# Kernel optimization log

Measured on AMD Instinct MI355X. Metric: run time of the kernel, lower is better.

The kernel has to match this reference:

```python
import jax, jax.numpy as jnp
import numpy as np

X_DIM = 64
Y_DIM = 64
U_DIM = 64
BATCH = 32
SEQ_LEN = 2048
DT = 1.0 / 1024.0
EPS = 1e-4


def setup_inputs() -> dict:
    key = jax.random.key(0)
    k_y, k_a, k_c = jax.random.split(key, 3)
    y = jax.random.normal(k_y, (BATCH, SEQ_LEN, Y_DIM), dtype=jnp.float32)
    # parameters, matching the module's initialization (small noise added to A/C for generality)
    A = jnp.diag(-0.01 * (jnp.arange(X_DIM, dtype=jnp.float32) + 1.0)) \
        + 0.001 * jax.random.normal(k_a, (X_DIM, X_DIM), dtype=jnp.float32)
    B = jnp.eye(X_DIM, U_DIM, dtype=jnp.float32) * 0.1
    C = 0.1 * jax.random.normal(k_c, (Y_DIM, X_DIM), dtype=jnp.float32)
    L_Q = jnp.eye(X_DIM, dtype=jnp.float32) * 0.316
    L_R = jnp.eye(U_DIM, dtype=jnp.float32) * 0.316
    L_V = jnp.eye(Y_DIM, dtype=jnp.float32)
    L_Q_proc = jnp.eye(X_DIM, dtype=jnp.float32) * 0.1
    x0_mean = jnp.zeros((X_DIM,), dtype=jnp.float32)
    P0 = jnp.eye(X_DIM, dtype=jnp.float32) * 0.1
    return {"y": y, "A": A, "B": B, "C": C, "L_Q": L_Q, "L_R": L_R,
            "L_V": L_V, "L_Q_proc": L_Q_proc, "x0_mean": x0_mean, "P0": P0}


def _riccati_step(S, H, n):
    # Euler step of the augmented Hamiltonian flow; P = V @ U^{-1}
    S_new = S + DT * (H @ S)
    U, V = S_new[:n], S_new[n:]
    X = V @ jnp.linalg.inv(U)
    return X, S_new


def _forward(y, A, B, C, L_Q, L_R, L_V, L_Q_proc, x0_mean, P0):
    n = A.shape[0]
    u_dim = B.shape[1]
    y_dim = C.shape[0]
    batch, seq_len, _ = y.shape

    Q = L_Q @ L_Q.T
    R = L_R @ L_R.T
    V = L_V @ L_V.T
    Q_proc = L_Q_proc @ L_Q_proc.T

    # normalize observations (torch.std is unbiased -> ddof=1)
    y_mean = y.mean(axis=(0, 1), keepdims=True)
    y_std = y.std(axis=(0, 1), keepdims=True, ddof=1)
    yn = (y - y_mean) / (y_std + EPS)

    # --- LQR Riccati recursion: P_seq, K_seq (sequential scan over time) ---
    R_inv_reg = jnp.linalg.inv(R + EPS * jnp.eye(u_dim, dtype=R.dtype))
    H_care = jnp.block([[A, -B @ jnp.linalg.inv(R) @ B.T],
                        [-Q, -A.T]])  # augmented Hamiltonian (2n, 2n)

    def lqr_step(S, _):
        X, S_new = _riccati_step(S, H_care, n)
        P = 0.5 * (X + X.T)
        K = R_inv_reg @ (B.T @ P)  # (u_dim, n)
        return S_new, (P, K)

    S0 = jnp.concatenate([jnp.eye(n, dtype=Q.dtype), Q], axis=0)  # P0 = Q
    _, (P_seq, K_seq) = jax.lax.scan(lqr_step, S0, None, length=seq_len)

    # --- Kalman filter (sequential scan, data-dependent per-step linear algebra) ---
    V_reg = V + EPS * jnp.eye(y_dim, dtype=V.dtype)
    V_chol = jnp.linalg.cholesky(V_reg)
    log_det_V = 2.0 * jnp.sum(jnp.log(jnp.diagonal(V_chol)))
    Z = jnp.zeros((n, n), dtype=A.dtype)
    LOG_2PI = jnp.log(2.0 * jnp.pi).astype(A.dtype)

    def kf_step(carry, inp):
        x_t, S, ll = carry
        K_t, y_t = inp  # (u_dim, n), (batch, y_dim)
        A_eff = A - B @ K_t
        x_pred = x_t + DT * (x_t @ A_eff.T)  # (batch, n)
        H_t = jnp.block([[A_eff, Q_proc], [Z, -A_eff.T]])
        P_new, S = _riccati_step(S, H_t, n)
        P_pred = 0.5 * (P_new + P_new.T)
        residual = y_t - x_pred @ C.T  # (batch, y_dim)
        CtP = C @ P_pred  # (y_dim, n)
        Sm = CtP @ C.T + V
        S_inv = jnp.linalg.inv(Sm + EPS * jnp.eye(y_dim, dtype=Sm.dtype))
        Kg = CtP.T @ S_inv  # (n, y_dim)
        x_new = x_pred + residual @ Kg.T
        quad = jnp.sum(residual * (residual @ S_inv.T))  # sum_b r^T S_inv r
        ll = ll - 0.5 * (quad + log_det_V + y_dim * LOG_2PI)
        return (x_new, S, ll), x_new

    S0_kf = jnp.concatenate([jnp.eye(n, dtype=P0.dtype), P0], axis=0)
    x0 = jnp.broadcast_to(x0_mean, (batch, n))
    y_t_major = jnp.swapaxes(yn, 0, 1)  # (T, B, y_dim)
    (_, _, ll), x_filt_t = jax.lax.scan(kf_step, (x0, S0_kf, jnp.float32(0.0)),
                                        (K_seq, y_t_major))
    x_filt = jnp.swapaxes(x_filt_t, 0, 1)  # (B, T, n)
    log_likelihood = ll / seq_len

    # controls, prediction, quadratic costs (fully vectorized)
    u_seq = -jnp.einsum('tux,btx->btu', K_seq, x_filt)
    y_pred = x_filt @ C.T
    x_cost = jnp.einsum('btx,xz,btz->b', x_filt, Q, x_filt)
    u_cost = jnp.einsum('btu,uv,btv->b', u_seq, R, u_seq)
    control_cost = jnp.mean(x_cost + u_cost)
    return log_likelihood, control_cost, x_filt, u_seq, y_pred, yn


def reference(y, A, B, C, L_Q, L_R, L_V, L_Q_proc, x0_mean, P0):
    return _forward(y, A, B, C, L_Q, L_R, L_V, L_Q_proc, x0_mean, P0)
```

## Files before the change

kernel.cpp:

```cpp
#include <hip/hip_runtime.h>
#include <math.h>

#define XD 64
#define SEQL 2048
#define NB 32
#define DT_C  (1.0f/1024.0f)
#define EPS_C 1e-4f
#define LD 68
#define PLD 136
#define LOG2PI 1.8378770664093453f
#define CHUNK 16
#define NCH 128

#define OFF_PARTIAL 0u
#define OFF_MEAN    32768u
#define OFF_STD     32832u
#define OFF_Q       32896u
#define OFF_R       36992u
#define OFF_VM      41088u
#define OFF_QP      45184u
#define OFF_RIREG   49280u
#define OFF_LOGDET  53376u
#define OFF_CHAIN   53440u
#define OFF_POW     250048u
#define OFF_BOUNDS  1298624u
#define OFF_K       1568960u
#define OFF_AEFF    9957568u
#define OFF_UV      18346176u
#define OFF_G       35123392u
#define OFF_B       43512000u
#define OFF_OPS2    47706304u
#define OFF_OPS3G   50852032u
#define OFF_OPS3B   51900608u
#define OFF_SB2     52424896u
#define OFF_XB      53473472u
#define OFF_QUAD    53735616u
#define OFF_COST    53737664u

#define OOFF_XF 2
#define OOFF_U  4194306
#define OOFF_YP 8388610
#define OOFF_YN 12582914

template<int KD>
__device__ __forceinline__ void mmNN(int t, float* __restrict__ out, int ldo,
    const float* __restrict__ A, int lda, const float* __restrict__ B, int ldb,
    const float* __restrict__ addC = nullptr, int ldc = 0, float alpha = 1.0f)
{
  const int r0 = (t >> 4) << 2, c0 = (t & 15) << 2;
  float acc[4][4] = {};
  for (int k = 0; k < KD; k += 4) {
    float a_[4][4];
    #pragma unroll
    for (int i = 0; i < 4; ++i) {
      const float4 x = *(const float4*)&A[(r0+i)*lda + k];
      a_[i][0]=x.x; a_[i][1]=x.y; a_[i][2]=x.z; a_[i][3]=x.w;
    }
    #pragma unroll
    for (int kk = 0; kk < 4; ++kk) {
      const float4 bv = *(const float4*)&B[(k+kk)*ldb + c0];
      #pragma unroll
      for (int i = 0; i < 4; ++i) {
        const float a = a_[i][kk];
        acc[i][0] += a*bv.x; acc[i][1] += a*bv.y; acc[i][2] += a*bv.z; acc[i][3] += a*bv.w;
      }
    }
  }
  #pragma unroll
  for (int i = 0; i < 4; ++i)
    #pragma unroll
    for (int j = 0; j < 4; ++j) {
      float v = alpha*acc[i][j];
      if (addC) v += addC[(r0+i)*ldc + (c0+j)];
      out[(r0+i)*ldo + (c0+j)] = v;
    }
}

template<int KD>
__device__ __forceinline__ void mmTA(int t, float* __restrict__ out, int ldo,
    const float* __restrict__ A, int lda, const float* __restrict__ B, int ldb,
    const float* __restrict__ addC = nullptr, int ldc = 0, float alpha = 1.0f)
{
  const int r0 = (t >> 4) << 2, c0 = (t & 15) << 2;
  float acc[4][4] = {};
  for (int k = 0; k < KD; k += 4) {
    #pragma unroll
    for (int kk = 0; kk < 4; ++kk) {
      const float4 av4 = *(const float4*)&A[(k+kk)*lda + r0];
      const float4 bv4 = *(const float4*)&B[(k+kk)*ldb + c0];
      const float av[4] = {av4.x, av4.y, av4.z, av4.w};
      const float bv[4] = {bv4.x, bv4.y, bv4.z, bv4.w};
      #pragma unroll
      for (int i = 0; i < 4; ++i)
        #pragma unroll
        for (int j = 0; j < 4; ++j)
          acc[i][j] += av[i]*bv[j];
    }
  }
  #pragma unroll
  for (int i = 0; i < 4; ++i)
    #pragma unroll
    for (int j = 0; j < 4; ++j) {
      float v = alpha*acc[i][j];
      if (addC) v += addC[(r0+i)*ldc + (c0+j)];
      out[(r0+i)*ldo + (c0+j)] = v;
    }
}

template<int KD>
__device__ __forceinline__ void mmTB(int t, float* __restrict__ out, int ldo,
    const float* __restrict__ A, int lda, const float* __restrict__ B, int ldb,
    const float* __restrict__ addC = nullptr, int ldc = 0, float alpha = 1.0f)
{
  const int r0 = (t >> 4) << 2, c0 = (t & 15) << 2;
  float acc[4][4] = {};
  for (int k = 0; k < KD; k += 4) {
    float a_[4][4], b_[4][4];
    #pragma unroll
    for (int i = 0; i < 4; ++i) {
      const float4 x = *(const float4*)&A[(r0+i)*lda + k];
      a_[i][0]=x.x; a_[i][1]=x.y; a_[i][2]=x.z; a_[i][3]=x.w;
    }
    #pragma unroll
    for (int j = 0; j < 4; ++j) {
      const float4 x = *(const float4*)&B[(c0+j)*ldb + k];
      b_[j][0]=x.x; b_[j][1]=x.y; b_[j][2]=x.z; b_[j][3]=x.w;
    }
    #pragma unroll
    for (int i = 0; i < 4; ++i)
      #pragma unroll
      for (int j = 0; j < 4; ++j)
        acc[i][j] += a_[i][0]*b_[j][0] + a_[i][1]*b_[j][1] + a_[i][2]*b_[j][2] + a_[i][3]*b_[j][3];
  }
  #pragma unroll
  for (int i = 0; i < 4; ++i)
    #pragma unroll
    for (int j = 0; j < 4; ++j) {
      float v = alpha*acc[i][j];
      if (addC) v += addC[(r0+i)*ldc + (c0+j)];
      out[(r0+i)*ldo + (c0+j)] = v;
    }
}

template<int KD>
__device__ __forceinline__ void mm32NN(int t, float* __restrict__ out, int ldo,
    const float* __restrict__ A, int lda, const float* __restrict__ B, int ldb,
    const float* __restrict__ addC = nullptr, int ldc = 0, float alpha = 1.0f)
{
  const int r0 = (t >> 4) << 1, c0 = (t & 15) << 2;
  float acc[2][4] = {};
  for (int k = 0; k < KD; k += 4) {
    float a_[2][4];
    #pragma unroll
    for (int i = 0; i < 2; ++i) {
      const float4 x = *(const float4*)&A[(r0+i)*lda + k];
      a_[i][0]=x.x; a_[i][1]=x.y; a_[i][2]=x.z; a_[i][3]=x.w;
    }
    #pragma unroll
    for (int kk = 0; kk < 4; ++kk) {
      const float4 bv = *(const float4*)&B[(k+kk)*ldb + c0];
      #pragma unroll
      for (int i = 0; i < 2; ++i) {
        const float a = a_[i][kk];
        acc[i][0] += a*bv.x; acc[i][1] += a*bv.y; acc[i][2] += a*bv.z; acc[i][3] += a*bv.w;
      }
    }
  }
  #pragma unroll
  for (int i = 0; i < 2; ++i)
    #pragma unroll
    for (int j = 0; j < 4; ++j) {
      float v = alpha*acc[i][j];
      if (addC) v += addC[(r0+i)*ldc + (c0+j)];
      out[(r0+i)*ldo + (c0+j)] = v;
    }
}

template<int KD>
__device__ __forceinline__ void mm32TB(int t, float* __restrict__ out, int ldo,
    const float* __restrict__ A, int lda, const float* __restrict__ B, int ldb,
    const float* __restrict__ addC = nullptr, int ldc = 0, float alpha = 1.0f)
{
  const int r0 = (t >> 4) << 1, c0 = (t & 15) << 2;
  float acc[2][4] = {};
  for (int k = 0; k < KD; k += 4) {
    float a_[2][4], b_[4][4];
    #pragma unroll
    for (int i = 0; i < 2; ++i) {
      const float4 x = *(const float4*)&A[(r0+i)*lda + k];
      a_[i][0]=x.x; a_[i][1]=x.y; a_[i][2]=x.z; a_[i][3]=x.w;
    }
    #pragma unroll
    for (int j = 0; j < 4; ++j) {
      const float4 x = *(const float4*)&B[(c0+j)*ldb + k];
      b_[j][0]=x.x; b_[j][1]=x.y; b_[j][2]=x.z; b_[j][3]=x.w;
    }
    #pragma unroll
    for (int i = 0; i < 2; ++i)
      #pragma unroll
      for (int j = 0; j < 4; ++j)
        acc[i][j] += a_[i][0]*b_[j][0] + a_[i][1]*b_[j][1] + a_[i][2]*b_[j][2] + a_[i][3]*b_[j][3];
  }
  #pragma unroll
  for (int i = 0; i < 2; ++i)
    #pragma unroll
    for (int j = 0; j < 4; ++j) {
      float v = alpha*acc[i][j];
      if (addC) v += addC[(r0+i)*ldc + (c0+j)];
      out[(r0+i)*ldo + (c0+j)] = v;
    }
}

__device__ __forceinline__ void gj64(int t, float* __restrict__ Am, float* __restrict__ R)
{
  const int r = t >> 2;
  const int c0 = (t & 3) << 4;
  for (int k = 0; k < 64; ++k) {
    __syncthreads();
    const float pv = Am[k*LD + k];
    const float f = Am[r*LD + k] / pv;
    if (r != k) {
      #pragma unroll
      for (int c = 0; c < 16; c += 4) {
        float4 ak = *(const float4*)&Am[k*LD + c0 + c];
        float4 ar = *(float4*)&Am[r*LD + c0 + c];
        ar.x -= f*ak.x; ar.y -= f*ak.y; ar.z -= f*ak.z; ar.w -= f*ak.w;
        *(float4*)&Am[r*LD + c0 + c] = ar;
        float4 rk = *(const float4*)&R[k*LD + c0 + c];
        float4 rr = *(float4*)&R[r*LD + c0 + c];
        rr.x -= f*rk.x; rr.y -= f*rk.y; rr.z -= f*rk.z; rr.w -= f*rk.w;
        *(float4*)&R[r*LD + c0 + c] = rr;
      }
    }
  }
  __syncthreads();
  const float dinv = 1.0f / Am[r*LD + r];
  #pragma unroll
  for (int c = 0; c < 16; c += 4) {
    float4 rr = *(float4*)&R[r*LD + c0 + c];
    rr.x *= dinv; rr.y *= dinv; rr.z *= dinv; rr.w *= dinv;
    *(float4*)&R[r*LD + c0 + c] = rr;
  }
  __syncthreads();
}

__device__ __forceinline__ void gjb8(int t, float* __restrict__ Am, float* __restrict__ R,
                                     float* __restrict__ pnl, float* __restrict__ w8)
{
  const int r  = t >> 2;
  const int c0 = (t & 3) << 4;
  const int j2 = t >> 5;
  const int cc = (t & 31) << 2;
  for (int kb = 0; kb < 8; ++kb) {
    const int K = kb << 3;
    __syncthreads();
    if (t < 64) {
      const int i = t >> 3, j = t & 7;
      float a = Am[(K+i)*LD + K + j];
      float w = (i == j) ? 1.0f : 0.0f;
      #pragma unroll
      for (int p = 0; p < 8; ++p) {
        const float pv  = __shfl(a, p*8 + p, 64);
        const float aip = __shfl(a, i*8 + p, 64);
        const float apj = __shfl(a, p*8 + j, 64);
        const float wpj = __shfl(w, p*8 + j, 64);
        const float fi  = aip / pv;
        if (i == p) { a = a / pv; w = w / pv; }
        else        { a -= fi * apj; w -= fi * wpj; }
      }
      w8[t] = w;
    }
    __syncthreads();
    {
      const int c4 = cc & 63;
      const float* srcB = (cc < 64) ? Am : R;
      const int off = (cc < 64) ? 0 : 68;
      float4 acc = make_float4(0.f, 0.f, 0.f, 0.f);
      #pragma unroll
      for (int m = 0; m < 8; ++m) {
        const float wv = w8[j2*8 + m];
        const float4 rv = *(const float4*)&srcB[(K+m)*LD + c4];
        acc.x += wv*rv.x; acc.y += wv*rv.y; acc.z += wv*rv.z; acc.w += wv*rv.w;
      }
      *(float4*)&pnl[j2*PLD + off + c4] = acc;
    }
    __syncthreads();
    {
      const float4 f0 = *(const float4*)&Am[r*LD + K];
      const float4 f1 = *(const float4*)&Am[r*LD + K + 4];
      const float fj[8] = {f0.x, f0.y, f0.z, f0.w, f1.x, f1.y, f1.z, f1.w};
      const bool inK = ((unsigned)(r - K)) < 8u;
      #pragma unroll
      for (int c = 0; c < 16; c += 4) {
        const int cab = c0 + c;
        if (cab >= K + 8) {
          float4 v;
          if (inK) {
            v = *(const float4*)&pnl[(r-K)*PLD + cab];
          } else {
            v = *(float4*)&Am[r*LD + cab];
            #pragma unroll
            for (int j = 0; j < 8; ++j) {
              const float4 p4 = *(const float4*)&pnl[j*PLD + cab];
              v.x -= fj[j]*p4.x; v.y -= fj[j]*p4.y; v.z -= fj[j]*p4.z; v.w -= fj[j]*p4.w;
            }
          }
          *(float4*)&Am[r*LD + cab] = v;
        }
      }
      #pragma unroll
      for (int c = 0; c < 16; c += 4) {
        const int cab = c0 + c;
        float4 v;
        if (inK) {
          v = *(const float4*)&pnl[(r-K)*PLD + 68 + cab];
        } else {
          v = *(float4*)&R[r*LD + cab];
          #pragma unroll
          for (int j = 0; j < 8; ++j) {
            const float4 p4 = *(const float4*)&pnl[j*PLD + 68 + cab];
            v.x -= fj[j]*p4.x; v.y -= fj[j]*p4.y; v.z -= fj[j]*p4.z; v.w -= fj[j]*p4.w;
          }
        }
        *(float4*)&R[r*LD + cab] = v;
      }
    }
  }
  __syncthreads();
}


__global__ __launch_bounds__(256) void k_stats(const float* __restrict__ y, float* __restrict__ ws)
{
  __shared__ float sbuf[4][128];
  const int t = threadIdx.x, blk = blockIdx.x;
  const int d = t & 63, g = t >> 6;
  float s = 0.f, s2 = 0.f;
  for (int r = g; r < 256; r += 4) {
    const float v = y[(size_t)(blk*256 + r)*64 + d];
    s += v; s2 += v*v;
  }
  sbuf[g][d] = s; sbuf[g][64+d] = s2;
  __syncthreads();
  if (t < 128) ws[OFF_PARTIAL + (size_t)blk*128 + t] = sbuf[0][t]+sbuf[1][t]+sbuf[2][t]+sbuf[3][t];
}

__global__ __launch_bounds__(256) void k_setup(
    const float* __restrict__ A, const float* __restrict__ Bi,
    const float* __restrict__ LQ, const float* __restrict__ LR,
    const float* __restrict__ LV, const float* __restrict__ LQp,
    float* __restrict__ ws)
{
  __shared__ float b1[64*LD], b2[64*LD], b3[64*LD], b4[64*LD], bQ[64*LD];
  __shared__ float sred[128];
  const int t = threadIdx.x;

  if (t < 128) {
    float acc = 0.f;
    for (int p = 0; p < 256; ++p) acc += ws[OFF_PARTIAL + (size_t)p*128 + t];
    sred[t] = acc;
  }
  __syncthreads();
  if (t < 64) {
    const float mean = sred[t] * (1.0f/65536.0f);
    const float var = (sred[64+t] - 65536.0f*mean*mean) * (1.0f/65535.0f);
    ws[OFF_MEAN + t] = mean;
    ws[OFF_STD + t] = sqrtf(var);
  }

  mmTB<64>(t, bQ, LD, LQ, 64, LQ, 64);
  mmTB<64>(t, b3, LD, LR, 64, LR, 64);
  mmTB<64>(t, ws+OFF_VM, 64, LV, 64, LV, 64);
  mmTB<64>(t, ws+OFF_QP, 64, LQp, 64, LQp, 64);
  __syncthreads();
  for (int idx = t; idx < 4096; idx += 256) {
    const int r = idx>>6, c = idx&63;
    ws[OFF_Q + idx] = bQ[r*LD+c];
    ws[OFF_R + idx] = b3[r*LD+c];
    b1[r*LD+c] = b3[r*LD+c] + ((r==c)?EPS_C:0.f);
    b2[r*LD+c] = (r==c)?1.f:0.f;
  }
  gj64(t, b1, b2);
  for (int idx = t; idx < 4096; idx += 256) ws[OFF_RIREG + idx] = b2[(idx>>6)*LD+(idx&63)];
  __syncthreads();
  for (int idx = t; idx < 4096; idx += 256) {
    const int r = idx>>6, c = idx&63;
    b1[r*LD+c] = b3[r*LD+c];
    b2[r*LD+c] = (r==c)?1.f:0.f;
  }
  gj64(t, b1, b2);
  mmTB<64>(t, b3, LD, b2, LD, Bi, 64);
  __syncthreads();
  mmNN<64>(t, b4, LD, Bi, 64, b3, LD);
  mmTB<64>(t, b1, LD, LV, 64, LV, 64);
  __syncthreads();
  if (t < 64) b1[t*LD+t] += EPS_C;
  {
    const int r = t >> 2, c0 = (t & 3) << 4;
    float lsum = 0.f;
    for (int k = 0; k < 64; ++k) {
      __syncthreads();
      const float pv = b1[k*LD+k];
      lsum += logf(pv);
      const float f = b1[r*LD+k] / pv;
      if (r != k) {
        #pragma unroll
        for (int c = 0; c < 16; c += 4) {
          float4 ak = *(const float4*)&b1[k*LD+c0+c];
          float4 ar = *(float4*)&b1[r*LD+c0+c];
          ar.x -= f*ak.x; ar.y -= f*ak.y; ar.z -= f*ak.z; ar.w -= f*ak.w;
          *(float4*)&b1[r*LD+c0+c] = ar;
        }
      }
    }
    if (t == 0) ws[OFF_LOGDET] = lsum;
  }
  __syncthreads();
  float* M0 = ws + OFF_CHAIN;
  for (int idx = t; idx < 16384; idx += 256) {
    const int i = idx >> 7, j = idx & 127;
    float v;
    if (i < 64) v = (j < 64) ? (((i==j)?1.f:0.f) + DT_C*A[i*64+j]) : (-DT_C*b4[i*LD + (j-64)]);
    else        v = (j < 64) ? (-DT_C*bQ[(i-64)*LD + j]) : (((i==j)?1.f:0.f) - DT_C*A[(j-64)*64 + (i-64)]);
    M0[idx] = v;
  }
  for (int idx = t; idx < 16384; idx += 256) {
    const int i = idx >> 7, j = idx & 127;
    ws[OFF_POW + idx] = (i==j)?1.f:0.f;
  }
  for (int idx = t; idx < 8192; idx += 256) {
    const int i = idx >> 6, j = idx & 63;
    ws[OFF_BOUNDS + idx] = (i < 64) ? ((i==j)?1.f:0.f) : bQ[(i-64)*LD + j];
  }
}

__global__ __launch_bounds__(256) void k_yn(const float* __restrict__ y, const float* __restrict__ ws, float* __restrict__ out)
{
  const size_t i0 = ((size_t)blockIdx.x*256 + threadIdx.x)*4;
  const int d = (int)(i0 & 63);
  const float4 v = *(const float4*)&y[i0];
  const float4 m = *(const float4*)&ws[OFF_MEAN + d];
  const float4 s = *(const float4*)&ws[OFF_STD + d];
  float* o = out + OOFF_YN + i0;
  o[0] = (v.x - m.x)/(s.x + EPS_C);
  o[1] = (v.y - m.y)/(s.y + EPS_C);
  o[2] = (v.z - m.z)/(s.z + EPS_C);
  o[3] = (v.w - m.w)/(s.w + EPS_C);
}

__global__ __launch_bounds__(256) void k_sq(const float* __restrict__ src, float* __restrict__ dst)
{
  const int t = threadIdx.x;
  const int r = blockIdx.x*8 + (t >> 5);
  const int c0 = (t & 31) << 2;
  float acc[4] = {0.f,0.f,0.f,0.f};
  for (int k = 0; k < 128; k += 4) {
    const float4 a4 = *(const float4*)&src[r*128 + k];
    const float av[4] = {a4.x, a4.y, a4.z, a4.w};
    #pragma unroll
    for (int kk = 0; kk < 4; ++kk) {
      const float4 bv = *(const float4*)&src[(k+kk)*128 + c0];
      acc[0] += av[kk]*bv.x; acc[1] += av[kk]*bv.y; acc[2] += av[kk]*bv.z; acc[3] += av[kk]*bv.w;
    }
  }
  float4 o; o.x=acc[0]; o.y=acc[1]; o.z=acc[2]; o.w=acc[3];
  *(float4*)&dst[r*128 + c0] = o;
}

__global__ __launch_bounds__(256) void k_pow(const float* __restrict__ chainj, float* __restrict__ powt, int level)
{
  const int i = blockIdx.x >> 2, sub = blockIdx.x & 3;
  const float* Bm = powt + (size_t)i*16384;
  float* D = powt + (size_t)(i + (1<<level))*16384;
  const int t = threadIdx.x;
  const int r0 = sub*32 + ((t >> 4) << 1);
  const int c0 = (t & 15) << 3;
  float acc[2][8] = {};
  for (int k = 0; k < 128; k += 4) {
    float a_[2][4];
    {
      const float4 x = *(const float4*)&chainj[r0*128 + k];
      a_[0][0]=x.x; a_[0][1]=x.y; a_[0][2]=x.z; a_[0][3]=x.w;
      const float4 y2 = *(const float4*)&chainj[(r0+1)*128 + k];
      a_[1][0]=y2.x; a_[1][1]=y2.y; a_[1][2]=y2.z; a_[1][3]=y2.w;
    }
    #pragma unroll
    for (int kk = 0; kk < 4; ++kk) {
      const float4 b0 = *(const float4*)&Bm[(k+kk)*128 + c0];
      const float4 b1v = *(const float4*)&Bm[(k+kk)*128 + c0 + 4];
      #pragma unroll
      for (int i2 = 0; i2 < 2; ++i2) {
        const float a = a_[i2][kk];
        acc[i2][0] += a*b0.x; acc[i2][1] += a*b0.y; acc[i2][2] += a*b0.z; acc[i2][3] += a*b0.w;
        acc[i2][4] += a*b1v.x; acc[i2][5] += a*b1v.y; acc[i2][6] += a*b1v.z; acc[i2][7] += a*b1v.w;
      }
    }
  }
  #pragma unroll
  for (int i2 = 0; i2 < 2; ++i2)
    #pragma unroll
    for (int j = 0; j < 8; ++j)
      D[(r0+i2)*128 + c0 + j] = acc[i2][j];
}

__global__ __launch_bounds__(256) void k_boundsk(const float* __restrict__ chainp, float* __restrict__ ws, int level)
{
  const int kb = blockIdx.x >> 1, sub = blockIdx.x & 1;
  const int dsti = kb + (1 << level);
  if (dsti > 32) return;
  const float* S = ws + OFF_BOUNDS + (size_t)kb*8192;
  float* D = ws + OFF_BOUNDS + (size_t)dsti*8192;
  const int t = threadIdx.x;
  const int r0 = sub*64 + ((t >> 4) << 2);
  const int c0 = (t & 15) << 2;
  float acc[4][4] = {};
  for (int k = 0; k < 128; k += 4) {
    float a_[4][4];
    #pragma unroll
    for (int i = 0; i < 4; ++i) {
      const float4 x = *(const float4*)&chainp[(r0+i)*128 + k];
      a_[i][0]=x.x; a_[i][1]=x.y; a_[i][2]=x.z; a_[i][3]=x.w;
    }
    #pragma unroll
    for (int kk = 0; kk < 4; ++kk) {
      const float4 bv = *(const float4*)&S[(k+kk)*64 + c0];
      #pragma unroll
      for (int i = 0; i < 4; ++i) {
        const float a = a_[i][kk];
        acc[i][0] += a*bv.x; acc[i][1] += a*bv.y; acc[i][2] += a*bv.z; acc[i][3] += a*bv.w;
      }
    }
  }
  #pragma unroll
  for (int i = 0; i < 4; ++i)
    #pragma unroll
    for (int j = 0; j < 4; ++j)
      D[(r0+i)*64 + c0 + j] = acc[i][j];
}

__global__ __launch_bounds__(256) void k_lqr(const float* __restrict__ Ain, const float* __restrict__ Bin, float* __restrict__ ws)
{
  __shared__ float b1[64*LD], b2[64*LD], b3[64*LD];
  __shared__ float pnl[8*PLD], w8[64];
  const int t = threadIdx.x, tt = blockIdx.x;
  const int tp1 = tt + 1, kc = tp1 >> 6, rr = tp1 & 63;
  const float* Mr = ws + OFF_POW + (size_t)rr*16384;
  const float* SB = ws + OFF_BOUNDS + (size_t)kc*8192;
  mmNN<128>(t, b1, LD, Mr, 128, SB, 64);
  mmNN<128>(t, b3, LD, Mr + 8192, 128, SB, 64);
  for (int idx = t; idx < 4096; idx += 256) {
    const int r = idx>>6, c = idx&63;
    b2[r*LD+c] = (r==c)?1.f:0.f;
  }
  gjb8(t, b1, b2, pnl, w8);
  mmNN<64>(t, b1, LD, b3, LD, b2, LD);
  __syncthreads();
  for (int idx = t; idx < 4096; idx += 256) {
    const int r = idx>>6, c = idx&63;
    b3[r*LD+c] = 0.5f*(b1[r*LD+c] + b1[c*LD+r]);
  }
  __syncthreads();
  mmTA<64>(t, b1, LD, Bin, 64, b3, LD);
  __syncthreads();
  mmNN<64>(t, b2, LD, ws+OFF_RIREG, 64, b1, LD);
  __syncthreads();
  float* Kout = ws + OFF_K + (size_t)tt*4096;
  for (int idx = t; idx < 4096; idx += 256) Kout[idx] = b2[(idx>>6)*LD+(idx&63)];
  mmNN<64>(t, b1, LD, Bin, 64, b2, LD);
  __syncthreads();
  float* Ae = ws + OFF_AEFF + (size_t)tt*4096;
  for (int idx = t; idx < 4096; idx += 256) Ae[idx] = Ain[idx] - b1[(idx>>6)*LD+(idx&63)];
}

__global__ __launch_bounds__(1024) void k_ops2(const float* __restrict__ ws_aeff, const float* __restrict__ ws_qp, float* __restrict__ dstE)
{
  __shared__ float E[64*LD], W[64*LD], F[64*LD], T1[64*LD], T2[64*LD], T3[64*LD], T4[64*LD];
  const int t = threadIdx.x, c = blockIdx.x, g = t >> 8, tl = t & 255;
  for (int idx = t; idx < 4096; idx += 1024) {
    const int r = idx>>6, cc = idx&63; const float id = (r==cc)?1.f:0.f;
    E[r*LD+cc] = id; W[r*LD+cc] = 0.f; F[r*LD+cc] = id;
  }
  __syncthreads();
  for (int s = 0; s < CHUNK; ++s) {
    const float* Ae = ws_aeff + ((size_t)c*CHUNK + s)*4096;
    if (g == 0)      mmNN<64>(tl, T1, LD, Ae, 64, E, LD);
    else if (g == 1) mmNN<64>(tl, T2, LD, Ae, 64, W, LD);
    else if (g == 2) mmNN<64>(tl, T3, LD, ws_qp, 64, F, LD);
    else             mmTA<64>(tl, T4, LD, Ae, 64, F, LD);
    __syncthreads();
    for (int idx = t; idx < 4096; idx += 1024) {
      const int p = (idx>>6)*LD + (idx&63);
      E[p] += DT_C*T1[p];
      W[p] += DT_C*(T2[p] + T3[p]);
      F[p] -= DT_C*T4[p];
    }
    __syncthreads();
  }
  float* dst = dstE + (size_t)c*12288;
  for (int idx = t; idx < 4096; idx += 1024) {
    const int p = (idx>>6)*LD + (idx&63);
    dst[idx] = E[p]; dst[4096+idx] = W[p]; dst[8192+idx] = F[p];
  }
}

__global__ __launch_bounds__(1024) void k_scan2(const float* __restrict__ src, float* __restrict__ dst, int s)
{
  __shared__ float t1[64*LD], t2[64*LD];
  const int i = blockIdx.x, t = threadIdx.x, g = t>>8, tl = t&255;
  const float* si = src + (size_t)i*12288;
  float* di = dst + (size_t)i*12288;
  if (i < s) {
    for (int idx = t; idx < 12288; idx += 1024) di[idx] = si[idx];
    return;
  }
  const float* sj = src + (size_t)(i-s)*12288;
  if (g == 0)      mmNN<64>(tl, di, 64, si, 64, sj, 64);
  else if (g == 1) mmNN<64>(tl, t1, LD, si, 64, sj+4096, 64);
  else if (g == 2) mmNN<64>(tl, t2, LD, si+4096, 64, sj+8192, 64);
  else             mmNN<64>(tl, di+8192, 64, si+8192, 64, sj+8192, 64);
  __syncthreads();
  for (int idx = t; idx < 4096; idx += 1024) {
    const int p = (idx>>6)*LD + (idx&63);
    di[4096+idx] = t1[p] + t2[p];
  }
}

__global__ __launch_bounds__(256) void k_sb2(const float* __restrict__ phi, const float* __restrict__ P0, float* __restrict__ ws)
{
  const int c = blockIdx.x, t = threadIdx.x;
  float* D = ws + OFF_SB2 + (size_t)c*8192;
  if (c == 0) {
    for (int idx = t; idx < 4096; idx += 256) {
      const int r = idx>>6, cc = idx&63;
      D[idx] = (r==cc)?1.f:0.f;
      D[4096+idx] = P0[idx];
    }
    return;
  }
  const float* ph = phi + (size_t)(c-1)*12288;
  mmNN<64>(t, D, 64, ph+4096, 64, P0, 64, ph, 64);
  mmNN<64>(t, D+4096, 64, ph+8192, 64, P0, 64);
}

__global__ __launch_bounds__(1024) void k_uvwalk(const float* __restrict__ ws_aeff, const float* __restrict__ ws_qp,
    const float* __restrict__ ws_sb2, float* __restrict__ ws_uv)
{
  __shared__ float U[64*LD], V[64*LD], T1[64*LD], T2[64*LD], T3[64*LD];
  const int c = blockIdx.x, t = threadIdx.x, g = t>>8, tl = t&255;
  const float* S = ws_sb2 + (size_t)c*8192;
  for (int idx = t; idx < 4096; idx += 1024) {
    const int p = (idx>>6)*LD + (idx&63);
    U[p] = S[idx]; V[p] = S[4096+idx];
  }
  __syncthreads();
  for (int s = 0; s < CHUNK; ++s) {
    const size_t tt = (size_t)c*CHUNK + s;
    const float* Ae = ws_aeff + tt*4096;
    if (g == 0)      mmNN<64>(tl, T1, LD, Ae, 64, U, LD);
    else if (g == 1) mmNN<64>(tl, T2, LD, ws_qp, 64, V, LD);
    else if (g == 2) mmTA<64>(tl, T3, LD, Ae, 64, V, LD);
    __syncthreads();
    float* O = ws_uv + tt*8192;
    for (int idx = t; idx < 4096; idx += 1024) {
      const int p = (idx>>6)*LD + (idx&63);
      const float un = U[p] + DT_C*(T1[p] + T2[p]);
      const float vn = V[p] - DT_C*T3[p];
      U[p] = un; V[p] = vn;
      O[idx] = un; O[4096+idx] = vn;
    }
    __syncthreads();
  }
}

__global__ __launch_bounds__(256) void k_kfper(const float* __restrict__ Cin, float* __restrict__ ws)
{
  __shared__ float b1[64*LD], b2[64*LD], b3[64*LD];
  __shared__ float pnl[8*PLD], w8[64];
  const int t = threadIdx.x, tt = blockIdx.x;
  float* base = ws + OFF_UV + (size_t)tt*8192;
  for (int idx = t; idx < 4096; idx += 256) {
    const int r = idx>>6, c = idx&63;
    b1[r*LD+c] = base[idx];
    b2[r*LD+c] = (r==c)?1.f:0.f;
  }
  gjb8(t, b1, b2, pnl, w8);
  mmNN<64>(t, b3, LD, base+4096, 64, b2, LD);
  __syncthreads();
  for (int idx = t; idx < 4096; idx += 256) {
    const int r = idx>>6, c = idx&63;
    b1[r*LD+c] = 0.5f*(b3[r*LD+c] + b3[c*LD+r]);
  }
  __syncthreads();
  mmNN<64>(t, b3, LD, Cin, 64, b1, LD);
  __syncthreads();
  mmTB<64>(t, b2, LD, b3, LD, Cin, 64, ws+OFF_VM, 64);
  __syncthreads();
  if (t < 64) b2[t*LD+t] += EPS_C;
  for (int idx = t; idx < 4096; idx += 256) {
    const int r = idx>>6, c = idx&63;
    b1[r*LD+c] = (r==c)?1.f:0.f;
  }
  gjb8(t, b2, b1, pnl, w8);
  for (int idx = t; idx < 4096; idx += 256) base[4096+idx] = b1[(idx>>6)*LD+(idx&63)];
  mmTA<64>(t, b2, LD, b3, LD, b1, LD);
  __syncthreads();
  for (int idx = t; idx < 4096; idx += 256) base[idx] = b2[(idx>>6)*LD+(idx&63)];
  mmNN<64>(t, b3, LD, b2, LD, Cin, 64);
  __syncthreads();
  const float* Ae = ws + OFF_AEFF + (size_t)tt*4096;
  float* Gg = ws + OFF_G + (size_t)tt*4096;
  {
    const int r0 = (t>>4)<<2, cg0 = (t&15)<<2;
    float acc[4][4] = {};
    for (int k = 0; k < 64; k += 4) {
      float a_[4][4];
      #pragma unroll
      for (int kk = 0; kk < 4; ++kk) {
        const float4 x = *(const float4*)&Ae[(k+kk)*64 + r0];
        a_[kk][0]=x.x; a_[kk][1]=x.y; a_[kk][2]=x.z; a_[kk][3]=x.w;
      }
      float yv[4][4];
      #pragma unroll
      for (int j = 0; j < 4; ++j) {
        const float4 z4 = *(const float4*)&b3[(cg0+j)*LD + k];
        yv[j][0] = -z4.x; yv[j][1] = -z4.y; yv[j][2] = -z4.z; yv[j][3] = -z4.w;
        const int dk = (cg0+j) - k;
        if (dk >= 0 && dk < 4) yv[j][dk] += 1.0f;
      }
      #pragma unroll
      for (int kk = 0; kk < 4; ++kk)
        #pragma unroll
        for (int i = 0; i < 4; ++i) {
          const float a = a_[kk][i];
          #pragma unroll
          for (int j = 0; j < 4; ++j) acc[i][j] += a * yv[j][kk];
        }
    }
    #pragma unroll
    for (int i = 0; i < 4; ++i)
      #pragma unroll
      for (int j = 0; j < 4; ++j) {
        const int rw = r0+i, cw = cg0+j;
        const float Yij = ((rw==cw)?1.f:0.f) - b3[cw*LD + rw];
        Gg[rw*64+cw] = Yij + DT_C*acc[i][j];
      }
  }
}

__global__ __launch_bounds__(256) void k_bvec(const float* __restrict__ outyn, float* __restrict__ ws)
{
  __shared__ float y32[NB*LD];
  const int tt = blockIdx.x, t = threadIdx.x;
  for (int idx = t; idx < 2048; idx += 256) {
    const int i = idx>>6, d = idx&63;
    y32[i*LD+d] = outyn[(size_t)i*131072 + (size_t)tt*64 + d];
  }
  __syncthreads();
  mm32TB<64>(t, ws + OFF_B + (size_t)tt*2048, 64, y32, LD, ws + OFF_UV + (size_t)tt*8192, 64);
}

__global__ __launch_bounds__(1024) void k_ops3(const float* __restrict__ ws_g, const float* __restrict__ ws_b,
    float* __restrict__ dG, float* __restrict__ dB)
{
  __shared__ float Gc[64*LD], TG[64*LD], bc[NB*LD], Tb[NB*LD];
  const int t = threadIdx.x, c = blockIdx.x, g = t >> 8, tl = t & 255;
  for (int idx = t; idx < 4096; idx += 1024) {
    const int r = idx>>6, cc = idx&63;
    Gc[r*LD+cc] = (r==cc)?1.f:0.f;
  }
  for (int idx = t; idx < 2048; idx += 1024) bc[(idx>>6)*LD+(idx&63)] = 0.f;
  __syncthreads();
  for (int s = 0; s < CHUNK; ++s) {
    const size_t tt = (size_t)c*CHUNK + s;
    const float* Gt = ws_g + tt*4096;
    if (g == 0)      mmNN<64>(tl, TG, LD, Gc, LD, Gt, 64);
    else if (g == 1) mm32NN<64>(tl, Tb, LD, bc, LD, Gt, 64);
    __syncthreads();
    for (int idx = t; idx < 4096; idx += 1024) {
      const int p = (idx>>6)*LD + (idx&63);
      Gc[p] = TG[p];
    }
    const float* bt = ws_b + tt*2048;
    for (int idx = t; idx < 2048; idx += 1024) {
      const int p = (idx>>6)*LD + (idx&63);
      bc[p] = Tb[p] + bt[idx];
    }
    __syncthreads();
  }
  for (int idx = t; idx < 4096; idx += 1024) dG[(size_t)c*4096 + idx] = Gc[(idx>>6)*LD+(idx&63)];
  for (int idx = t; idx < 2048; idx += 1024) dB[(size_t)c*2048 + idx] = bc[(idx>>6)*LD+(idx&63)];
}

__global__ __launch_bounds__(512) void k_scan3(const float* __restrict__ sG, const float* __restrict__ sB,
    float* __restrict__ dG, float* __restrict__ dB, int s)
{
  const int i = blockIdx.x, t = threadIdx.x, g = t>>8, tl = t&255;
  if (i < s) {
    for (int idx = t; idx < 4096; idx += 512) dG[(size_t)i*4096+idx] = sG[(size_t)i*4096+idx];
    for (int idx = t; idx < 2048; idx += 512) dB[(size_t)i*2048+idx] = sB[(size_t)i*2048+idx];
    return;
  }
  const float* Ge = sG + (size_t)(i-s)*4096;
  const float* Gl = sG + (size_t)i*4096;
  if (g == 0) mmNN<64>(tl, dG + (size_t)i*4096, 64, Ge, 64, Gl, 64);
  else        mm32NN<64>(tl, dB + (size_t)i*2048, 64, sB + (size_t)(i-s)*2048, 64, Gl, 64,
                         sB + (size_t)i*2048, 64);
}

__global__ __launch_bounds__(256) void k_xb(const float* __restrict__ phiG, const float* __restrict__ phiB,
    const float* __restrict__ x0, float* __restrict__ ws)
{
  __shared__ float v[64];
  const int c = blockIdx.x, t = threadIdx.x;
  float* D = ws + OFF_XB + (size_t)c*2048;
  if (c == 0) {
    for (int idx = t; idx < 2048; idx += 256) D[idx] = x0[idx&63];
    return;
  }
  const float* G = phiG + (size_t)(c-1)*4096;
  const float* b = phiB + (size_t)(c-1)*2048;
  if (t < 64) {
    float acc = 0.f;
    for (int k = 0; k < 64; ++k) acc += x0[k]*G[k*64 + t];
    v[t] = acc;
  }
  __syncthreads();
  for (int idx = t; idx < 2048; idx += 256) D[idx] = v[idx&63] + b[idx];
}

__global__ __launch_bounds__(256) void k_xwalk(const float* __restrict__ ws_g, const float* __restrict__ ws_b,
    const float* __restrict__ ws_xb, float* __restrict__ outx)
{
  __shared__ float x[NB*LD], xn[NB*LD];
  const int c = blockIdx.x, t = threadIdx.x;
  const float* X0 = ws_xb + (size_t)c*2048;
  for (int idx = t; idx < 2048; idx += 256) x[(idx>>6)*LD+(idx&63)] = X0[idx];
  __syncthreads();
  for (int s = 0; s < CHUNK; ++s) {
    const size_t tt = (size_t)c*CHUNK + s;
    mm32NN<64>(t, xn, LD, x, LD, ws_g + tt*4096, 64, ws_b + tt*2048, 64);
    __syncthreads();
    for (int idx = t; idx < 2048; idx += 256) {
      const int i = idx>>6, d = idx&63;
      const float val = xn[i*LD+d];
      x[i*LD+d] = val;
      outx[(size_t)i*131072 + tt*64 + d] = val;
    }
    __syncthreads();
  }
}

__global__ __launch_bounds__(256) void k_final(const float* __restrict__ Cin, const float* __restrict__ x0,
    const float* __restrict__ outx, const float* __restrict__ outyn,
    float* __restrict__ outu, float* __restrict__ outyp, float* __restrict__ ws)
{
  __shared__ float xc[NB*LD], z[NB*LD], t1[NB*LD], t2[NB*LD];
  __shared__ float red4[4];
  const int tt = blockIdx.x, t = threadIdx.x;
  for (int idx = t; idx < 2048; idx += 256) {
    const int i = idx>>6, d = idx&63;
    xc[i*LD+d] = outx[(size_t)i*131072 + (size_t)tt*64 + d];
    z[i*LD+d]  = (tt == 0) ? x0[d] : outx[(size_t)i*131072 + (size_t)(tt-1)*64 + d];
  }
  __syncthreads();
  mm32TB<64>(t, t1, LD, xc, LD, ws + OFF_K + (size_t)tt*4096, 64, nullptr, 0, -1.0f);
  mm32TB<64>(t, t2, LD, xc, LD, Cin, 64);
  __syncthreads();
  for (int idx = t; idx < 2048; idx += 256) {
    const int i = idx>>6, d = idx&63;
    outu[(size_t)i*131072 + (size_t)tt*64 + d]  = t1[i*LD+d];
    outyp[(size_t)i*131072 + (size_t)tt*64 + d] = t2[i*LD+d];
  }
  __syncthreads();
  mm32NN<64>(t, t2, LD, xc, LD, ws + OFF_Q, 64);
  __syncthreads();
  const int i_ = t >> 3, lane8 = t & 7;
  float cpart = 0.f;
  for (int d = lane8; d < 64; d += 8) cpart += t2[i_*LD+d]*xc[i_*LD+d];
  __syncthreads();
  mm32NN<64>(t, t2, LD, t1, LD, ws + OFF_R, 64);
  __syncthreads();
  for (int d = lane8; d < 64; d += 8) cpart += t2[i_*LD+d]*t1[i_*LD+d];
  cpart += __shfl_down(cpart, 4, 8);
  cpart += __shfl_down(cpart, 2, 8);
  cpart += __shfl_down(cpart, 1, 8);
  if (lane8 == 0) ws[OFF_COST + (size_t)tt*32 + i_] = cpart;
  __syncthreads();
  mm32TB<64>(t, t2, LD, z, LD, ws + OFF_AEFF + (size_t)tt*4096, 64, z, LD, DT_C);
  __syncthreads();
  mm32TB<64>(t, t1, LD, t2, LD, Cin, 64, outyn + (size_t)tt*64, 131072, -1.0f);
  __syncthreads();
  mm32TB<64>(t, z, LD, t1, LD, ws + OFF_UV + (size_t)tt*8192 + 4096, 64);
  __syncthreads();
  float q = 0.f;
  for (int idx = t; idx < 2048; idx += 256) {
    const int p = (idx>>6)*LD + (idx&63);
    q += t1[p]*z[p];
  }
  q += __shfl_down(q, 32); q += __shfl_down(q, 16); q += __shfl_down(q, 8);
  q += __shfl_down(q, 4);  q += __shfl_down(q, 2);  q += __shfl_down(q, 1);
  if ((t & 63) == 0) red4[t>>6] = q;
  __syncthreads();
  if (t == 0) ws[OFF_QUAD + tt] = red4[0]+red4[1]+red4[2]+red4[3];
}

__global__ __launch_bounds__(256) void k_scalars(const float* __restrict__ ws, float* __restrict__ out)
{
  __shared__ float red[256];
  const int t = threadIdx.x;
  float q = 0.f;
  for (int i = t; i < 2048; i += 256) q += ws[OFF_QUAD + i];
  red[t] = q;
  __syncthreads();
  for (int s = 128; s > 0; s >>= 1) { if (t < s) red[t] += red[t+s]; __syncthreads(); }
  const float quadsum = red[0];
  __syncthreads();
  {
    const int b = t & 31, chunk = t >> 5;
    float a = 0.f;
    for (int j = 0; j < 256; ++j) a += ws[OFF_COST + (size_t)(chunk*256 + j)*32 + b];
    red[t] = a;
  }
  __syncthreads();
  if (t < 32) {
    float a = 0.f;
    for (int ch = 0; ch < 8; ++ch) a += red[ch*32 + t];
    red[t] = a;
  }
  __syncthreads();
  if (t == 0) {
    float cc = 0.f;
    for (int b = 0; b < 32; ++b) cc += red[b];
    out[1] = cc / 32.0f;
    const float ld = ws[OFF_LOGDET];
    out[0] = -0.5f*(quadsum + 2048.0f*(ld + 64.0f*LOG2PI)) / 2048.0f;
  }
}

extern "C" void kernel_launch(void* const* d_in, const int* in_sizes, int n_in,
                              void* d_out, int out_size, void* d_ws, size_t ws_size,
                              hipStream_t stream)
{
  (void)in_sizes; (void)n_in; (void)out_size; (void)ws_size;
  const float* y   = (const float*)d_in[0];
  const float* A   = (const float*)d_in[1];
  const float* Bi  = (const float*)d_in[2];
  const float* C   = (const float*)d_in[3];
  const float* LQ  = (const float*)d_in[4];
  const float* LR  = (const float*)d_in[5];
  const float* LV  = (const float*)d_in[6];
  const float* LQp = (const float*)d_in[7];
  const float* x0  = (const float*)d_in[8];
  const float* P0  = (const float*)d_in[9];
  float* out = (float*)d_out;
  float* ws  = (float*)d_ws;

  k_stats<<<256, 256, 0, stream>>>(y, ws);
  k_setup<<<1, 256, 0, stream>>>(A, Bi, LQ, LR, LV, LQp, ws);
  k_yn<<<4096, 256, 0, stream>>>(y, ws, out);

  for (int j = 1; j <= 11; ++j)
    k_sq<<<16, 256, 0, stream>>>(ws + OFF_CHAIN + (size_t)(j-1)*16384, ws + OFF_CHAIN + (size_t)j*16384);
  for (int j = 0; j <= 5; ++j)
    k_pow<<<4 << j, 256, 0, stream>>>(ws + OFF_CHAIN + (size_t)j*16384, ws + OFF_POW, j);
  for (int j = 0; j <= 5; ++j)
    k_boundsk<<<2 << j, 256, 0, stream>>>(ws + OFF_CHAIN + (size_t)(6+j)*16384, ws, j);

  k_lqr<<<2048, 256, 0, stream>>>(A, Bi, ws);

  k_ops2<<<NCH, 1024, 0, stream>>>(ws + OFF_AEFF, ws + OFF_QP, ws + OFF_OPS2);
  {
    float* pa = ws + OFF_OPS2;
    float* pb = pa + (size_t)NCH*12288;
    float* src = pa; float* dst = pb;
    for (int s = 1; s < NCH; s <<= 1) {
      k_scan2<<<NCH, 1024, 0, stream>>>(src, dst, s);
      float* tmp = src; src = dst; dst = tmp;
    }
    k_sb2<<<NCH, 256, 0, stream>>>(src, P0, ws);
  }
  k_uvwalk<<<NCH, 1024, 0, stream>>>(ws + OFF_AEFF, ws + OFF_QP, ws + OFF_SB2, ws + OFF_UV);
  k_kfper<<<2048, 256, 0, stream>>>(C, ws);

  k_bvec<<<2048, 256, 0, stream>>>(out + OOFF_YN, ws);
  k_ops3<<<NCH, 1024, 0, stream>>>(ws + OFF_G, ws + OFF_B, ws + OFF_OPS3G, ws + OFF_OPS3B);
  {
    float* ga = ws + OFF_OPS3G; float* gb = ga + (size_t)NCH*4096;
    float* ba = ws + OFF_OPS3B; float* bb = ba + (size_t)NCH*2048;
    float *gs = ga, *gd = gb, *bs = ba, *bd = bb;
    for (int s = 1; s < NCH; s <<= 1) {
      k_scan3<<<NCH, 512, 0, stream>>>(gs, bs, gd, bd, s);
      float* t1p = gs; gs = gd; gd = t1p;
      float* t2p = bs; bs = bd; bd = t2p;
    }
    k_xb<<<NCH, 256, 0, stream>>>(gs, bs, x0, ws);
  }
  k_xwalk<<<NCH, 256, 0, stream>>>(ws + OFF_G, ws + OFF_B, ws + OFF_XB, out + OOFF_XF);

  k_final<<<2048, 256, 0, stream>>>(C, x0, out + OOFF_XF, out + OOFF_YN, out + OOFF_U, out + OOFF_YP, ws);
  k_scalars<<<1, 256, 0, stream>>>(ws, out);
}
```

Baseline: 2.542 ms.

## Drop panel buffer in blocked Gauss-Jordan, fuse bvec into kfper, raise occupancy

The blocked Gauss-Jordan inverse now writes the scaled pivot block rows back into the matrix in place instead of staging them in a separate shared panel buffer. This removes the panel's shared memory so three blocks can fit per CU, and launch bounds request that. The k_bvec kernel is folded into k_kfper, which reads yn directly from global memory with a 64-bit stride and uses the inverse still held in shared memory, saving a launch and a global reload. The in-place update needs an extra barrier per pivot block and reads strided global memory for the B vector.

Measured after the change: 3.331 ms. 31.1% more time.

```diff
diff --git a/kernel.cpp b/kernel.cpp
--- a/kernel.cpp
+++ b/kernel.cpp
@@ -7,7 +7,6 @@
 #define DT_C  (1.0f/1024.0f)
 #define EPS_C 1e-4f
 #define LD 68
-#define PLD 136
 #define LOG2PI 1.8378770664093453f
 #define CHUNK 16
 #define NCH 128
@@ -178,8 +177,8 @@
 
 template<int KD>
 __device__ __forceinline__ void mm32TB(int t, float* __restrict__ out, int ldo,
-    const float* __restrict__ A, int lda, const float* __restrict__ B, int ldb,
-    const float* __restrict__ addC = nullptr, int ldc = 0, float alpha = 1.0f)
+    const float* __restrict__ A, size_t lda, const float* __restrict__ B, int ldb,
+    const float* __restrict__ addC = nullptr, size_t ldc = 0, float alpha = 1.0f)
 {
   const int r0 = (t >> 4) << 1, c0 = (t & 15) << 2;
   float acc[2][4] = {};
@@ -187,7 +186,7 @@
     float a_[2][4], b_[4][4];
     #pragma unroll
     for (int i = 0; i < 2; ++i) {
-      const float4 x = *(const float4*)&A[(r0+i)*lda + k];
+      const float4 x = *(const float4*)&A[(size_t)(r0+i)*lda + k];
       a_[i][0]=x.x; a_[i][1]=x.y; a_[i][2]=x.z; a_[i][3]=x.w;
     }
     #pragma unroll
@@ -206,7 +205,7 @@
     #pragma unroll
     for (int j = 0; j < 4; ++j) {
       float v = alpha*acc[i][j];
-      if (addC) v += addC[(r0+i)*ldc + (c0+j)];
+      if (addC) v += addC[(size_t)(r0+i)*ldc + (c0+j)];
       out[(r0+i)*ldo + (c0+j)] = v;
     }
 }
@@ -245,7 +244,7 @@
 }
 
 __device__ __forceinline__ void gjb8(int t, float* __restrict__ Am, float* __restrict__ R,
-                                     float* __restrict__ pnl, float* __restrict__ w8)
+                                     float* __restrict__ w8)
 {
   const int r  = t >> 2;
   const int c0 = (t & 3) << 4;
@@ -271,39 +270,32 @@
       w8[t] = w;
     }
     __syncthreads();
-    {
-      const int c4 = cc & 63;
-      const float* srcB = (cc < 64) ? Am : R;
-      const int off = (cc < 64) ? 0 : 68;
-      float4 acc = make_float4(0.f, 0.f, 0.f, 0.f);
-      #pragma unroll
-      for (int m = 0; m < 8; ++m) {
-        const float wv = w8[j2*8 + m];
-        const float4 rv = *(const float4*)&srcB[(K+m)*LD + c4];
-        acc.x += wv*rv.x; acc.y += wv*rv.y; acc.z += wv*rv.z; acc.w += wv*rv.w;
-      }
-      *(float4*)&pnl[j2*PLD + off + c4] = acc;
-    }
-    __syncthreads();
-    {
+    const int c4 = cc & 63;
+    float* srcB = (cc < 64) ? Am : R;
+    float4 acc = make_float4(0.f, 0.f, 0.f, 0.f);
+    #pragma unroll
+    for (int m = 0; m < 8; ++m) {
+      const float wv = w8[j2*8 + m];
+      const float4 rv = *(const float4*)&srcB[(K+m)*LD + c4];
+      acc.x += wv*rv.x; acc.y += wv*rv.y; acc.z += wv*rv.z; acc.w += wv*rv.w;
+    }
+    __syncthreads();
+    *(float4*)&srcB[(K+j2)*LD + c4] = acc;
+    __syncthreads();
+    const bool inK = ((unsigned)(r - K)) < 8u;
+    if (!inK) {
       const float4 f0 = *(const float4*)&Am[r*LD + K];
       const float4 f1 = *(const float4*)&Am[r*LD + K + 4];
       const float fj[8] = {f0.x, f0.y, f0.z, f0.w, f1.x, f1.y, f1.z, f1.w};
-      const bool inK = ((unsigned)(r - K)) < 8u;
       #pragma unroll
       for (int c = 0; c < 16; c += 4) {
         const int cab = c0 + c;
         if (cab >= K + 8) {
-          float4 v;
-          if (inK) {
-            v = *(const float4*)&pnl[(r-K)*PLD + cab];
-          } else {
-            v = *(float4*)&Am[r*LD + cab];
-            #pragma unroll
-            for (int j = 0; j < 8; ++j) {
-              const float4 p4 = *(const float4*)&pnl[j*PLD + cab];
-              v.x -= fj[j]*p4.x; v.y -= fj[j]*p4.y; v.z -= fj[j]*p4.z; v.w -= fj[j]*p4.w;
-            }
+          float4 v = *(float4*)&Am[r*LD + cab];
+          #pragma unroll
+          for (int j = 0; j < 8; ++j) {
+            const float4 p4 = *(const float4*)&Am[(K+j)*LD + cab];
+            v.x -= fj[j]*p4.x; v.y -= fj[j]*p4.y; v.z -= fj[j]*p4.z; v.w -= fj[j]*p4.w;
           }
           *(float4*)&Am[r*LD + cab] = v;
         }
@@ -311,16 +303,11 @@
       #pragma unroll
       for (int c = 0; c < 16; c += 4) {
         const int cab = c0 + c;
-        float4 v;
-        if (inK) {
-          v = *(const float4*)&pnl[(r-K)*PLD + 68 + cab];
-        } else {
-          v = *(float4*)&R[r*LD + cab];
-          #pragma unroll
-          for (int j = 0; j < 8; ++j) {
-            const float4 p4 = *(const float4*)&pnl[j*PLD + 68 + cab];
-            v.x -= fj[j]*p4.x; v.y -= fj[j]*p4.y; v.z -= fj[j]*p4.z; v.w -= fj[j]*p4.w;
-          }
+        float4 v = *(float4*)&R[r*LD + cab];
+        #pragma unroll
+        for (int j = 0; j < 8; ++j) {
+          const float4 p4 = *(const float4*)&R[(K+j)*LD + cab];
+          v.x -= fj[j]*p4.x; v.y -= fj[j]*p4.y; v.z -= fj[j]*p4.z; v.w -= fj[j]*p4.w;
         }
         *(float4*)&R[r*LD + cab] = v;
       }
@@ -538,10 +525,10 @@
       D[(r0+i)*64 + c0 + j] = acc[i][j];
 }
 
-__global__ __launch_bounds__(256) void k_lqr(const float* __restrict__ Ain, const float* __restrict__ Bin, float* __restrict__ ws)
+__global__ __launch_bounds__(256, 3) void k_lqr(const float* __restrict__ Ain, const float* __restrict__ Bin, float* __restrict__ ws)
 {
   __shared__ float b1[64*LD], b2[64*LD], b3[64*LD];
-  __shared__ float pnl[8*PLD], w8[64];
+  __shared__ float w8[64];
   const int t = threadIdx.x, tt = blockIdx.x;
   const int tp1 = tt + 1, kc = tp1 >> 6, rr = tp1 & 63;
   const float* Mr = ws + OFF_POW + (size_t)rr*16384;
@@ -552,7 +539,7 @@
     const int r = idx>>6, c = idx&63;
     b2[r*LD+c] = (r==c)?1.f:0.f;
   }
-  gjb8(t, b1, b2, pnl, w8);
+  gjb8(t, b1, b2, w8);
   mmNN<64>(t, b1, LD, b3, LD, b2, LD);
   __syncthreads();
   for (int idx = t; idx < 4096; idx += 256) {
@@ -672,10 +659,10 @@
   }
 }
 
-__global__ __launch_bounds__(256) void k_kfper(const float* __restrict__ Cin, float* __restrict__ ws)
+__global__ __launch_bounds__(256, 3) void k_kfper(const float* __restrict__ Cin, const float* __restrict__ outyn, float* __restrict__ ws)
 {
   __shared__ float b1[64*LD], b2[64*LD], b3[64*LD];
-  __shared__ float pnl[8*PLD], w8[64];
+  __shared__ float w8[64];
   const int t = threadIdx.x, tt = blockIdx.x;
   float* base = ws + OFF_UV + (size_t)tt*8192;
   for (int idx = t; idx < 4096; idx += 256) {
@@ -683,7 +670,7 @@
     b1[r*LD+c] = base[idx];
     b2[r*LD+c] = (r==c)?1.f:0.f;
   }
-  gjb8(t, b1, b2, pnl, w8);
+  gjb8(t, b1, b2, w8);
   mmNN<64>(t, b3, LD, base+4096, 64, b2, LD);
   __syncthreads();
   for (int idx = t; idx < 4096; idx += 256) {
@@ -700,7 +687,7 @@
     const int r = idx>>6, c = idx&63;
     b1[r*LD+c] = (r==c)?1.f:0.f;
   }
-  gjb8(t, b2, b1, pnl, w8);
+  gjb8(t, b2, b1, w8);
   for (int idx = t; idx < 4096; idx += 256) base[4096+idx] = b1[(idx>>6)*LD+(idx&63)];
   mmTA<64>(t, b2, LD, b3, LD, b1, LD);
   __syncthreads();
@@ -745,18 +732,8 @@
         Gg[rw*64+cw] = Yij + DT_C*acc[i][j];
       }
   }
-}
-
-__global__ __launch_bounds__(256) void k_bvec(const float* __restrict__ outyn, float* __restrict__ ws)
-{
-  __shared__ float y32[NB*LD];
-  const int tt = blockIdx.x, t = threadIdx.x;
-  for (int idx = t; idx < 2048; idx += 256) {
-    const int i = idx>>6, d = idx&63;
-    y32[i*LD+d] = outyn[(size_t)i*131072 + (size_t)tt*64 + d];
-  }
-  __syncthreads();
-  mm32TB<64>(t, ws + OFF_B + (size_t)tt*2048, 64, y32, LD, ws + OFF_UV + (size_t)tt*8192, 64);
+  mm32TB<64>(t, ws + OFF_B + (size_t)tt*2048, 64,
+             outyn + (size_t)tt*64, (size_t)131072, b2, LD);
 }
 
 __global__ __launch_bounds__(1024) void k_ops3(const float* __restrict__ ws_g, const float* __restrict__ ws_b,
@@ -850,7 +827,7 @@
   }
 }
 
-__global__ __launch_bounds__(256) void k_final(const float* __restrict__ Cin, const float* __restrict__ x0,
+__global__ __launch_bounds__(256, 3) void k_final(const float* __restrict__ Cin, const float* __restrict__ x0,
     const float* __restrict__ outx, const float* __restrict__ outyn,
     float* __restrict__ outu, float* __restrict__ outyp, float* __restrict__ ws)
 {
@@ -888,7 +865,7 @@
   __syncthreads();
   mm32TB<64>(t, t2, LD, z, LD, ws + OFF_AEFF + (size_t)tt*4096, 64, z, LD, DT_C);
   __syncthreads();
-  mm32TB<64>(t, t1, LD, t2, LD, Cin, 64, outyn + (size_t)tt*64, 131072, -1.0f);
+  mm32TB<64>(t, t1, LD, t2, LD, Cin, 64, outyn + (size_t)tt*64, (size_t)131072, -1.0f);
   __syncthreads();
   mm32TB<64>(t, z, LD, t1, LD, ws + OFF_UV + (size_t)tt*8192 + 4096, 64);
   __syncthreads();
@@ -980,9 +957,8 @@
     k_sb2<<<NCH, 256, 0, stream>>>(src, P0, ws);
   }
   k_uvwalk<<<NCH, 1024, 0, stream>>>(ws + OFF_AEFF, ws + OFF_QP, ws + OFF_SB2, ws + OFF_UV);
-  k_kfper<<<2048, 256, 0, stream>>>(C, ws);
-
-  k_bvec<<<2048, 256, 0, stream>>>(out + OOFF_YN, ws);
+  k_kfper<<<2048, 256, 0, stream>>>(C, out + OOFF_YN, ws);
+
   k_ops3<<<NCH, 1024, 0, stream>>>(ws + OFF_G, ws + OFF_B, ws + OFF_OPS3G, ws + OFF_OPS3B);
   {
     float* ga = ws + OFF_OPS3G; float* gb = ga + (size_t)NCH*4096;
```
